# Performance work log

Measured on AMD Instinct MI355X. Metric: run time of the kernel, lower is better.

The kernel has to match this reference:

```python
import jax, jax.numpy as jnp
import numpy as np
import math

QUERY_DIM = 512
FEAT_DIM = 2048
HID_DIM = 512
OUT_DIM = 512
B, L, S, T = 32, 128, 36, 36


def _linear_params(key, d_in, d_out):
    kw, kb = jax.random.split(key)
    scale = 1.0 / math.sqrt(d_in)
    W = jax.random.uniform(kw, (d_in, d_out), jnp.float32, -scale, scale)
    b = jax.random.uniform(kb, (d_out,), jnp.float32, -scale, scale)
    return W, b


def setup_inputs() -> dict:
    key = jax.random.key(0)
    ks = jax.random.split(key, 9)
    query = jax.random.normal(ks[0], (B, L, QUERY_DIM), jnp.float32)
    src = jax.random.normal(ks[1], (B, S, FEAT_DIM), jnp.float32)
    trg = jax.random.normal(ks[2], (B, T, FEAT_DIM), jnp.float32)
    Wq, bq = _linear_params(ks[3], QUERY_DIM, HID_DIM)
    Ws, bs = _linear_params(ks[4], FEAT_DIM, HID_DIM)
    Wt, bt = _linear_params(ks[5], FEAT_DIM, HID_DIM)
    Wsv, bsv = _linear_params(ks[6], FEAT_DIM, HID_DIM)
    Wtv, btv = _linear_params(ks[7], FEAT_DIM, HID_DIM)
    Wo, bo = _linear_params(ks[8], HID_DIM * 2 + QUERY_DIM, OUT_DIM)
    return dict(query=query, src=src, trg=trg,
                Wq=Wq, bq=bq, Ws=Ws, bs=bs, Wt=Wt, bt=bt,
                Wsv=Wsv, bsv=bsv, Wtv=Wtv, btv=btv, Wo=Wo, bo=bo)


def reference(query, src, trg, Wq, bq, Ws, bs, Wt, bt, Wsv, bsv, Wtv, btv, Wo, bo):
    b, l, _ = query.shape
    s = src.shape[1]
    t = trg.shape[1]
    q = query @ Wq + bq                      # (b, l, h)
    s_key = src @ Ws + bs                    # (b, s, h)
    t_key = trg @ Wt + bt                    # (b, t, h)
    # Faithful to torch: s_key.unsqueeze(1) + t_key.unsqueeze(2) -> (b, t, s, h),
    # then labeled 'istk' in the einsum (requires s == t).
    rel_key = (s_key[:, None, :, :] + t_key[:, :, None, :]) * 0.5  # (b, t, s, h)
    weight = jnp.einsum('blk,bstk->blst', q, rel_key) / math.sqrt(HID_DIM)
    weight = jax.nn.softmax(weight.reshape(b, l, s * t), axis=-1).reshape(b, l, s, t)
    s_value = src @ Wsv + bsv                # (b, s, h)
    t_value = trg @ Wtv + btv                # (b, t, h)
    s_ctx = jnp.einsum('blst,bsh->blh', weight, s_value)
    t_ctx = jnp.einsum('blst,bth->blh', weight, t_value)
    x = jnp.concatenate((query, s_ctx, t_ctx), axis=-1)
    return jax.nn.relu(x @ Wo + bo)
```

## Files before the change

### kernel.cpp

```cpp
#include <hip/hip_runtime.h>
#include <hip/hip_bf16.h>
#include <math.h>

#define DEVI __device__ __forceinline__

typedef __attribute__((ext_vector_type(4))) float f32x4;
typedef __attribute__((ext_vector_type(8))) short bf16x8;

DEVI unsigned short f2bf(float f) {
  union { float f; unsigned int u; } v; v.f = f;
  return (unsigned short)((v.u + 0x7FFFu + ((v.u >> 16) & 1u)) >> 16);
}
DEVI float bf2f(unsigned short s) {
  union { unsigned int u; float f; } v; v.u = ((unsigned int)s) << 16; return v.f;
}
DEVI bf16x8 pack8(f32x4 a, f32x4 b) {
  bf16x8 r;
  r[0] = (short)f2bf(a[0]); r[1] = (short)f2bf(a[1]);
  r[2] = (short)f2bf(a[2]); r[3] = (short)f2bf(a[3]);
  r[4] = (short)f2bf(b[0]); r[5] = (short)f2bf(b[1]);
  r[6] = (short)f2bf(b[2]); r[7] = (short)f2bf(b[3]);
  return r;
}
DEVI void gload16(const unsigned short* g, unsigned short* l) {
  __builtin_amdgcn_global_load_lds(
      (const __attribute__((address_space(1))) unsigned int*)g,
      (__attribute__((address_space(3))) unsigned int*)l, 16, 0, 0);
}
#define SBAR() do { asm volatile("" ::: "memory"); \
                    __builtin_amdgcn_s_barrier();  \
                    asm volatile("" ::: "memory"); } while (0)

struct PrepJobs {
  const float* src[9];
  unsigned short* dst[9];
  int K[9];
  int base[9];
  int type[9];
};

__global__ __launch_bounds__(256) void prep(PrepJobs J) {
  __shared__ float t[64][65];
  int tile = blockIdx.x;
  int job = 0;
  while (job < 8 && tile >= J.base[job + 1]) ++job;
  int tl = tile - J.base[job];
  int K = J.K[job];
  if (J.type[job] == 0) {
    int tn = tl & 7, tk = tl >> 3;
    int x = threadIdx.x & 63, y = threadIdx.x >> 6;
    const float* s = J.src[job];
    int k0 = tk * 64, n0 = tn * 64;
#pragma unroll
    for (int yy = y; yy < 64; yy += 4)
      t[yy][x] = s[(size_t)(k0 + yy) * 512 + n0 + x];
    __syncthreads();
    unsigned short* d = J.dst[job];
    int kb = (x >> 3) & 7, ko = x & 7;
#pragma unroll
    for (int yy = y; yy < 64; yy += 4) {
      int n = n0 + yy;
      int kswz = k0 + (((kb + n) & 7) << 3) + ko;
      d[(size_t)n * K + kswz] = f2bf(t[x][yy]);
    }
  } else {
    int nk = K >> 6;
    int rt = tl / nk;
    int r0 = rt * 64, k0 = (tl - rt * nk) * 64;
    int r = threadIdx.x >> 2, kq = threadIdx.x & 3;
    int row = r0 + r;
    const float* s = J.src[job] + (size_t)row * K + k0 + kq * 16;
    f32x4 a0 = *(const f32x4*)s;
    f32x4 a1 = *(const f32x4*)(s + 4);
    f32x4 a2 = *(const f32x4*)(s + 8);
    f32x4 a3 = *(const f32x4*)(s + 12);
    unsigned short* d = J.dst[job] + (size_t)row * K + k0;
    int kb0 = kq * 2;
    *(bf16x8*)(d + ((kb0 + row) & 7) * 8) = pack8(a0, a1);
    *(bf16x8*)(d + ((kb0 + 1 + row) & 7) * 8) = pack8(a2, a3);
  }
}

struct GJob {
  const unsigned short* A0;
  const unsigned short* Bt;
  const float* bias;
  unsigned short* Cb;
  int Astride, Bstride, Cstride, nTilesN, nt, mode, tileBase;
};
struct GBatch { GJob j[7]; int njobs; int swz; };

__global__ __launch_bounds__(512) void gemm_pipe8(GBatch batch) {
  int gt = blockIdx.x;
  if (batch.swz) {
    int cpx = gridDim.x >> 3;
    gt = (blockIdx.x & 7) * cpx + (blockIdx.x >> 3);
  }
  int job = 0;
#pragma unroll
  for (int i = 1; i < 7; ++i)
    if (i < batch.njobs && gt >= batch.j[i].tileBase) job = i;
  GJob J = batch.j[job];
  int tl = gt - J.tileBase;
  int bm = (tl / J.nTilesN) * 128, bn = (tl % J.nTilesN) * 128;

  __shared__ __align__(16) unsigned short La[2][128 * 64];
  __shared__ __align__(16) unsigned short Lb[2][128 * 64];

  int tid = threadIdx.x;
  int wave = tid >> 6, lane = tid & 63;
  int lrow = lane & 15, lq = lane >> 4;
  int wr = (wave >> 1) * 32, wc = (wave & 1) * 64;
  f32x4 acc[2][4] = {};

  int nt = J.nt;

  auto stage_both = [&](int t, int buf) {
    const unsigned short* GA = J.A0 + (size_t)bm * J.Astride + (size_t)(t << 6);
    const unsigned short* GB = J.Bt + (size_t)bn * J.Bstride + (size_t)(t << 6);
#pragma unroll
    for (int p = 0; p < 2; ++p) {
      int s = p * 512 + tid;
      gload16(GA + (size_t)(s >> 3) * J.Astride + (s & 7) * 8,
              &La[buf][(size_t)(p * 512 + wave * 64) * 8]);
    }
#pragma unroll
    for (int p = 0; p < 2; ++p) {
      int s = p * 512 + tid;
      gload16(GB + (size_t)(s >> 3) * J.Bstride + (s & 7) * 8,
              &Lb[buf][(size_t)(p * 512 + wave * 64) * 8]);
    }
  };

  stage_both(0, 0);
  if (nt > 1) stage_both(1, 1);

  for (int t = 0; t < nt; ++t) {
    if (t + 1 < nt) asm volatile("s_waitcnt vmcnt(4)" ::: "memory");
    else            asm volatile("s_waitcnt vmcnt(0)" ::: "memory");
    SBAR();
    int cur = t & 1;
#pragma unroll
    for (int kc = 0; kc < 2; ++kc) {
      int kb = kc * 4 + lq;
      bf16x8 af[2], bv[4];
#pragma unroll
      for (int mi = 0; mi < 2; ++mi) {
        int r = wr + mi * 16 + lrow;
        af[mi] = *(const bf16x8*)&La[cur][r * 64 + ((kb + r) & 7) * 8];
      }
#pragma unroll
      for (int ni = 0; ni < 4; ++ni) {
        int r = wc + ni * 16 + lrow;
        bv[ni] = *(const bf16x8*)&Lb[cur][r * 64 + ((kb + r) & 7) * 8];
      }
#pragma unroll
      for (int mi = 0; mi < 2; ++mi)
#pragma unroll
        for (int ni = 0; ni < 4; ++ni)
          acc[mi][ni] = __builtin_amdgcn_mfma_f32_16x16x32_bf16(af[mi], bv[ni], acc[mi][ni], 0, 0, 0);
    }
    SBAR();
    if (t + 2 < nt) stage_both(t + 2, cur);
  }

#pragma unroll
  for (int mi = 0; mi < 2; ++mi) {
#pragma unroll
    for (int ni = 0; ni < 4; ++ni) {
      int gn = bn + wc + ni * 16 + lrow;
      float bvs = J.bias ? J.bias[gn] : 0.f;
      int gm0 = bm + wr + mi * 16 + lq * 4;
      if (J.mode == 0) {
#pragma unroll
        for (int r = 0; r < 4; ++r)
          J.Cb[(size_t)(gm0 + r) * J.Cstride + gn] = f2bf(acc[mi][ni][r] + bvs);
      } else {
#pragma unroll
        for (int r = 0; r < 4; ++r) {
          int row = gm0 + r;
          int col = (gn & ~63) | (((((gn >> 3) & 7) + row) & 7) << 3) | (gn & 7);
          J.Cb[(size_t)row * J.Cstride + col] = f2bf(acc[mi][ni][r] + bvs);
        }
      }
    }
  }
}

template <int MI, int NI>
__global__ __launch_bounds__(256) void gemm_pipe(GBatch batch) {
  constexpr int BM = MI * 32, BN = NI * 32;
  int gt = blockIdx.x;
  if (batch.swz) {
    int cpx = gridDim.x >> 3;
    gt = (blockIdx.x & 7) * cpx + (blockIdx.x >> 3);
  }
  int job = 0;
#pragma unroll
  for (int i = 1; i < 7; ++i)
    if (i < batch.njobs && gt >= batch.j[i].tileBase) job = i;
  GJob J = batch.j[job];
  int tl = gt - J.tileBase;
  int bm = (tl / J.nTilesN) * BM, bn = (tl % J.nTilesN) * BN;

  __shared__ __align__(16) unsigned short La[2][BM * 64];
  __shared__ __align__(16) unsigned short Lb[2][BN * 64];

  int tid = threadIdx.x;
  int wave = tid >> 6, lane = tid & 63;
  int lrow = lane & 15, lq = lane >> 4;
  int wr = (wave >> 1) * (MI * 16), wc = (wave & 1) * (NI * 16);
  f32x4 acc[MI][NI] = {};

  int nt = J.nt;

  auto stage_both = [&](int t, int buf) {
    const unsigned short* GA = J.A0 + (size_t)bm * J.Astride + (size_t)(t << 6);
    const unsigned short* GB = J.Bt + (size_t)bn * J.Bstride + (size_t)(t << 6);
#pragma unroll
    for (int p = 0; p < MI; ++p) {
      int s = p * 256 + tid;
      gload16(GA + (size_t)(s >> 3) * J.Astride + (s & 7) * 8,
              &La[buf][(size_t)(p * 256 + wave * 64) * 8]);
    }
#pragma unroll
    for (int p = 0; p < NI; ++p) {
      int s = p * 256 + tid;
      gload16(GB + (size_t)(s >> 3) * J.Bstride + (s & 7) * 8,
              &Lb[buf][(size_t)(p * 256 + wave * 64) * 8]);
    }
  };

  stage_both(0, 0);
  if (nt > 1) stage_both(1, 1);

  for (int t = 0; t < nt; ++t) {
    if (t + 1 < nt) {
      if constexpr (MI + NI == 8)      asm volatile("s_waitcnt vmcnt(8)" ::: "memory");
      else if constexpr (MI + NI == 6) asm volatile("s_waitcnt vmcnt(6)" ::: "memory");
      else                             asm volatile("s_waitcnt vmcnt(4)" ::: "memory");
    } else {
      asm volatile("s_waitcnt vmcnt(0)" ::: "memory");
    }
    SBAR();
    int cur = t & 1;
#pragma unroll
    for (int kc = 0; kc < 2; ++kc) {
      int kb = kc * 4 + lq;
      bf16x8 af[MI], bv[NI];
#pragma unroll
      for (int mi = 0; mi < MI; ++mi) {
        int r = wr + mi * 16 + lrow;
        af[mi] = *(const bf16x8*)&La[cur][r * 64 + ((kb + r) & 7) * 8];
      }
#pragma unroll
      for (int ni = 0; ni < NI; ++ni) {
        int r = wc + ni * 16 + lrow;
        bv[ni] = *(const bf16x8*)&Lb[cur][r * 64 + ((kb + r) & 7) * 8];
      }
#pragma unroll
      for (int mi = 0; mi < MI; ++mi)
#pragma unroll
        for (int ni = 0; ni < NI; ++ni)
          acc[mi][ni] = __builtin_amdgcn_mfma_f32_16x16x32_bf16(af[mi], bv[ni], acc[mi][ni], 0, 0, 0);
    }
    SBAR();
    if (t + 2 < nt) stage_both(t + 2, cur);
  }

#pragma unroll
  for (int mi = 0; mi < MI; ++mi) {
#pragma unroll
    for (int ni = 0; ni < NI; ++ni) {
      int gn = bn + wc + ni * 16 + lrow;
      float bvs = J.bias ? J.bias[gn] : 0.f;
      int gm0 = bm + wr + mi * 16 + lq * 4;
      if (J.mode == 0) {
#pragma unroll
        for (int r = 0; r < 4; ++r)
          J.Cb[(size_t)(gm0 + r) * J.Cstride + gn] = f2bf(acc[mi][ni][r] + bvs);
      } else {
#pragma unroll
        for (int r = 0; r < 4; ++r) {
          int row = gm0 + r;
          int col = (gn & ~63) | (((((gn >> 3) & 7) + row) & 7) << 3) | (gn & 7);
          J.Cb[(size_t)row * J.Cstride + col] = f2bf(acc[mi][ni][r] + bvs);
        }
      }
    }
  }
}

__global__ __launch_bounds__(256) void attn_fused(
    const unsigned short* __restrict__ qh, const unsigned short* __restrict__ s_key,
    const unsigned short* __restrict__ t_key, const unsigned short* __restrict__ svp,
    const unsigned short* __restrict__ tvp, const unsigned short* __restrict__ Pb,
    float* __restrict__ out) {
  __shared__ float red[4][3][64][4];
  __shared__ float wlT[2][36][16];
  int b = blockIdx.x, lc = blockIdx.y;
  int tid = threadIdx.x, wave = tid >> 6, lane = tid & 63;
  int lrow = lane & 15, lq = lane >> 4;
  int mat = wave >> 1, kh = wave & 1;
  int row0 = b * 128 + lc * 16;
  const unsigned short* qp = qh + (size_t)row0 * 512;
  const unsigned short* key = (mat ? s_key : t_key) + (size_t)b * 36 * 512;
  f32x4 acc[3] = {};
  for (int kc = kh * 8; kc < kh * 8 + 8; ++kc) {
    int k = kc * 32 + lq * 8;
    bf16x8 af = *(const bf16x8*)(qp + (size_t)lrow * 512 + k);
#pragma unroll
    for (int nf = 0; nf < 3; ++nf) {
      int n = nf * 16 + lrow; if (n > 35) n = 35;
      bf16x8 bv = *(const bf16x8*)(key + (size_t)n * 512 + k);
      acc[nf] = __builtin_amdgcn_mfma_f32_16x16x32_bf16(af, bv, acc[nf], 0, 0, 0);
    }
  }
#pragma unroll
  for (int nf = 0; nf < 3; ++nf)
    *(f32x4*)&red[wave][nf][lane][0] = acc[nf];
  __syncthreads();

  if (kh == 0) {
    const float ccs = 0.022097086912079608f;
    float ex[3][4];
#pragma unroll
    for (int r = 0; r < 4; ++r) {
      float a0 = (red[wave][0][lane][r] + red[wave + 1][0][lane][r]) * ccs;
      float a1 = (red[wave][1][lane][r] + red[wave + 1][1][lane][r]) * ccs;
      float a2 = (lrow < 4)
          ? (red[wave][2][lane][r] + red[wave + 1][2][lane][r]) * ccs : -1e30f;
      float mx = fmaxf(fmaxf(a0, a1), a2);
      for (int s = 1; s < 16; s <<= 1) mx = fmaxf(mx, __shfl_xor(mx, s));
      float e0 = __expf(a0 - mx), e1 = __expf(a1 - mx);
      float e2 = (lrow < 4) ? __expf(a2 - mx) : 0.f;
      float sum = e0 + e1 + e2;
      for (int s = 1; s < 16; s <<= 1) sum += __shfl_xor(sum, s);
      float inv = 1.f / sum;
      ex[0][r] = e0 * inv; ex[1][r] = e1 * inv; ex[2][r] = e2 * inv;
    }
#pragma unroll
    for (int nf = 0; nf < 3; ++nf) {
      int col = nf * 16 + lrow;
      if (col < 36) {
#pragma unroll
        for (int r = 0; r < 4; ++r)
          wlT[mat][col][lq * 4 + r] = ex[nf][r];
      }
    }
  }
  __syncthreads();

  int lgrp = tid >> 6, hgrp = tid & 63;
  float a2[4][8] = {};
#pragma unroll
  for (int m = 0; m < 2; ++m) {
    const unsigned short* V = (m ? tvp : svp) + (size_t)b * 36 * 512;
    for (int j = 0; j < 36; ++j) {
      f32x4 wa = *(const f32x4*)&wlT[m][j][lgrp * 4];
      bf16x8 v = *(const bf16x8*)(V + (size_t)j * 512 + hgrp * 8);
      float vf[8];
#pragma unroll
      for (int hi = 0; hi < 8; ++hi) vf[hi] = bf2f((unsigned short)v[hi]);
#pragma unroll
      for (int li = 0; li < 4; ++li)
#pragma unroll
        for (int hi = 0; hi < 8; ++hi) a2[li][hi] += wa[li] * vf[hi];
    }
  }
#pragma unroll
  for (int li = 0; li < 4; ++li) {
    int R = row0 + lgrp * 4 + li;
    bf16x8 p = *(const bf16x8*)(Pb + (size_t)R * 512 + hgrp * 8);
    float* op = out + (size_t)R * 512 + hgrp * 8;
    f32x4 o0, o1;
#pragma unroll
    for (int hi = 0; hi < 4; ++hi) {
      o0[hi] = fmaxf(bf2f((unsigned short)p[hi]) + a2[li][hi], 0.f);
      o1[hi] = fmaxf(bf2f((unsigned short)p[4 + hi]) + a2[li][4 + hi], 0.f);
    }
    *(f32x4*)op = o0;
    *(f32x4*)(op + 4) = o1;
  }
}

extern "C" void kernel_launch(void* const* d_in, const int* in_sizes, int n_in,
                              void* d_out, int out_size, void* d_ws, size_t ws_size,
                              hipStream_t stream) {
  (void)in_sizes; (void)n_in; (void)out_size; (void)ws_size;
  const float* query = (const float*)d_in[0];
  const float* src   = (const float*)d_in[1];
  const float* trg   = (const float*)d_in[2];
  const float* Wq  = (const float*)d_in[3];  const float* bq  = (const float*)d_in[4];
  const float* Wsk = (const float*)d_in[5];  const float* bs  = (const float*)d_in[6];
  const float* Wtk = (const float*)d_in[7];  const float* bt  = (const float*)d_in[8];
  const float* Wsv = (const float*)d_in[9];  const float* bsv = (const float*)d_in[10];
  const float* Wtv = (const float*)d_in[11]; const float* btv = (const float*)d_in[12];
  const float* Wo  = (const float*)d_in[13]; const float* bo  = (const float*)d_in[14];

  unsigned short* WqT    = (unsigned short*)d_ws;
  unsigned short* WsT    = WqT  + 512 * 512;
  unsigned short* WtT    = WsT  + 512 * 2048;
  unsigned short* WsvT   = WtT  + 512 * 2048;
  unsigned short* WtvT   = WsvT + 512 * 2048;
  unsigned short* WoT    = WtvT + 512 * 2048;
  unsigned short* queryB = WoT  + 512 * 1536;
  unsigned short* srcB   = queryB + 4096 * 512;
  unsigned short* trgB   = srcB + 1152 * 2048;
  unsigned short* qh     = trgB + 1152 * 2048;
  unsigned short* s_key  = qh + 4096 * 512;
  unsigned short* t_key  = s_key + 1152 * 512;
  unsigned short* s_val  = t_key + 1152 * 512;
  unsigned short* t_val  = s_val + 1152 * 512;
  unsigned short* svp    = t_val + 1152 * 512;
  unsigned short* tvp    = svp + 1152 * 512;
  unsigned short* Pb     = tvp + 1152 * 512;
  float* out = (float*)d_out;

  PrepJobs pj;
  const float* psrc[9] = { Wq, Wsk, Wtk, Wsv, Wtv, Wo, query, src, trg };
  unsigned short* pdst[9] = { WqT, WsT, WtT, WsvT, WtvT, WoT, queryB, srcB, trgB };
  int pK[9]    = { 512, 2048, 2048, 2048, 2048, 1536, 512, 2048, 2048 };
  int ptype[9] = { 0, 0, 0, 0, 0, 0, 1, 1, 1 };
  int prows[9] = { 0, 0, 0, 0, 0, 0, 4096, 1152, 1152 };
  int pbase = 0;
  for (int i = 0; i < 9; ++i) {
    pj.src[i] = psrc[i]; pj.dst[i] = pdst[i]; pj.K[i] = pK[i]; pj.type[i] = ptype[i];
    pj.base[i] = pbase;
    pbase += ptype[i] ? (prows[i] / 64) * (pK[i] / 64) : (pK[i] / 64) * 8;
  }
  prep<<<pbase, 256, 0, stream>>>(pj);

  {
    GBatch pb;
    pb.swz = 0;
    int base = 0;
    const unsigned short* Aarr[4] = { srcB, trgB, srcB, trgB };
    const unsigned short* Barr[4] = { WsT, WtT, WsvT, WtvT };
    const float* biasArr[4] = { bs, bt, bsv, btv };
    unsigned short* Carr[4] = { s_key, t_key, s_val, t_val };
    for (int i = 0; i < 4; ++i) {
      GJob& j = pb.j[i];
      j.A0 = Aarr[i]; j.Bt = Barr[i]; j.bias = biasArr[i]; j.Cb = Carr[i];
      j.Astride = 2048; j.Bstride = 2048; j.Cstride = 512;
      j.nTilesN = 4; j.nt = 32; j.mode = (i < 2) ? 0 : 2;
      j.tileBase = base; base += 9 * 4;
    }
    {
      GJob& j = pb.j[4];
      j.A0 = queryB; j.Bt = WqT; j.bias = bq; j.Cb = qh;
      j.Astride = 512; j.Bstride = 512; j.Cstride = 512;
      j.nTilesN = 4; j.nt = 8; j.mode = 0;
      j.tileBase = base; base += 32 * 4;
    }
    {
      GJob& j = pb.j[5];
      j.A0 = queryB; j.Bt = WoT; j.bias = bo; j.Cb = Pb;
      j.Astride = 512; j.Bstride = 1536; j.Cstride = 512;
      j.nTilesN = 4; j.nt = 8; j.mode = 0;
      j.tileBase = base; base += 32 * 4;
    }
    pb.j[6] = pb.j[5]; pb.j[6].tileBase = 0x7fffffff;
    pb.njobs = 6;
    gemm_pipe8<<<base, 512, 0, stream>>>(pb);
  }

  {
    GBatch sb;
    sb.swz = 1;
    GJob& a = sb.j[0];
    a.A0 = s_val; a.Bt = WoT + 512; a.bias = nullptr; a.Cb = svp;
    a.Astride = 512; a.Bstride = 1536; a.Cstride = 512;
    a.nTilesN = 8; a.nt = 8; a.mode = 0; a.tileBase = 0;
    GJob& b2 = sb.j[1];
    b2 = a;
    b2.A0 = t_val; b2.Bt = WoT + 1024; b2.Cb = tvp;
    b2.tileBase = 18 * 8;
    for (int i = 2; i < 7; ++i) { sb.j[i] = b2; sb.j[i].tileBase = 0x7fffffff; }
    sb.njobs = 2;
    gemm_pipe<2, 2><<<288, 256, 0, stream>>>(sb);
  }

  attn_fused<<<dim3(32, 8), 256, 0, stream>>>(qh, s_key, t_key, svp, tvp, Pb, out);
}
```

Baseline: 75.84 us.

## Fuse fp32-to-bf16 activation conversion into GEMM and split attention scoring into stage3

Drops the separate prep pass that converted query/src/trg to swizzled bf16. The projection GEMM now loads fp32 activations into registers, converts them and writes them to LDS, using 64-row tiles with 256 threads. The score/softmax part of the attention kernel moves into a combined launch alongside the value-by-Wo GEMM, writing softmax weights to a workspace for a separate weighted-sum kernel. This saves a full round trip of activation conversion traffic and overlaps the scoring with the small GEMM, at the cost of register-staged A loads and an extra fp32 weights buffer.

```diff
diff --git a/kernel.cpp b/kernel.cpp
--- a/kernel.cpp
+++ b/kernel.cpp
@@ -32,79 +32,57 @@
                     asm volatile("" ::: "memory"); } while (0)
 
 struct PrepJobs {
-  const float* src[9];
-  unsigned short* dst[9];
-  int K[9];
-  int base[9];
-  int type[9];
+  const float* src[6];
+  unsigned short* dst[6];
+  int K[6];
+  int base[6];
 };
 
 __global__ __launch_bounds__(256) void prep(PrepJobs J) {
   __shared__ float t[64][65];
   int tile = blockIdx.x;
   int job = 0;
-  while (job < 8 && tile >= J.base[job + 1]) ++job;
+  while (job < 5 && tile >= J.base[job + 1]) ++job;
   int tl = tile - J.base[job];
   int K = J.K[job];
-  if (J.type[job] == 0) {
-    int tn = tl & 7, tk = tl >> 3;
-    int x = threadIdx.x & 63, y = threadIdx.x >> 6;
-    const float* s = J.src[job];
-    int k0 = tk * 64, n0 = tn * 64;
-#pragma unroll
-    for (int yy = y; yy < 64; yy += 4)
-      t[yy][x] = s[(size_t)(k0 + yy) * 512 + n0 + x];
-    __syncthreads();
-    unsigned short* d = J.dst[job];
-    int kb = (x >> 3) & 7, ko = x & 7;
-#pragma unroll
-    for (int yy = y; yy < 64; yy += 4) {
-      int n = n0 + yy;
-      int kswz = k0 + (((kb + n) & 7) << 3) + ko;
-      d[(size_t)n * K + kswz] = f2bf(t[x][yy]);
-    }
-  } else {
-    int nk = K >> 6;
-    int rt = tl / nk;
-    int r0 = rt * 64, k0 = (tl - rt * nk) * 64;
-    int r = threadIdx.x >> 2, kq = threadIdx.x & 3;
-    int row = r0 + r;
-    const float* s = J.src[job] + (size_t)row * K + k0 + kq * 16;
-    f32x4 a0 = *(const f32x4*)s;
-    f32x4 a1 = *(const f32x4*)(s + 4);
-    f32x4 a2 = *(const f32x4*)(s + 8);
-    f32x4 a3 = *(const f32x4*)(s + 12);
-    unsigned short* d = J.dst[job] + (size_t)row * K + k0;
-    int kb0 = kq * 2;
-    *(bf16x8*)(d + ((kb0 + row) & 7) * 8) = pack8(a0, a1);
-    *(bf16x8*)(d + ((kb0 + 1 + row) & 7) * 8) = pack8(a2, a3);
-  }
-}
-
-struct GJob {
-  const unsigned short* A0;
+  int tn = tl & 7, tk = tl >> 3;
+  int x = threadIdx.x & 63, y = threadIdx.x >> 6;
+  const float* s = J.src[job];
+  int k0 = tk * 64, n0 = tn * 64;
+#pragma unroll
+  for (int yy = y; yy < 64; yy += 4)
+    t[yy][x] = s[(size_t)(k0 + yy) * 512 + n0 + x];
+  __syncthreads();
+  unsigned short* d = J.dst[job];
+  int kb = (x >> 3) & 7, ko = x & 7;
+#pragma unroll
+  for (int yy = y; yy < 64; yy += 4) {
+    int n = n0 + yy;
+    int kswz = k0 + (((kb + n) & 7) << 3) + ko;
+    d[(size_t)n * K + kswz] = f2bf(t[x][yy]);
+  }
+}
+
+struct PJob {
+  const float* Af;
   const unsigned short* Bt;
   const float* bias;
   unsigned short* Cb;
   int Astride, Bstride, Cstride, nTilesN, nt, mode, tileBase;
 };
-struct GBatch { GJob j[7]; int njobs; int swz; };
-
-__global__ __launch_bounds__(512) void gemm_pipe8(GBatch batch) {
+struct PBatch { PJob j[7]; int njobs; };
+
+__global__ __launch_bounds__(256, 3) void gemm_f32a(PBatch batch) {
   int gt = blockIdx.x;
-  if (batch.swz) {
-    int cpx = gridDim.x >> 3;
-    gt = (blockIdx.x & 7) * cpx + (blockIdx.x >> 3);
-  }
   int job = 0;
 #pragma unroll
   for (int i = 1; i < 7; ++i)
     if (i < batch.njobs && gt >= batch.j[i].tileBase) job = i;
-  GJob J = batch.j[job];
+  PJob J = batch.j[job];
   int tl = gt - J.tileBase;
-  int bm = (tl / J.nTilesN) * 128, bn = (tl % J.nTilesN) * 128;
-
-  __shared__ __align__(16) unsigned short La[2][128 * 64];
+  int bm = (tl / J.nTilesN) * 64, bn = (tl % J.nTilesN) * 128;
+
+  __shared__ __align__(16) unsigned short La[2][64 * 64];
   __shared__ __align__(16) unsigned short Lb[2][128 * 64];
 
   int tid = threadIdx.x;
@@ -113,32 +91,38 @@
   int wr = (wave >> 1) * 32, wc = (wave & 1) * 64;
   f32x4 acc[2][4] = {};
 
+  int row_a = tid >> 2, kq = tid & 3;
+  const float* Abase = J.Af + (size_t)(bm + row_a) * J.Astride + kq * 16;
   int nt = J.nt;
 
-  auto stage_both = [&](int t, int buf) {
-    const unsigned short* GA = J.A0 + (size_t)bm * J.Astride + (size_t)(t << 6);
+  f32x4 R[2][4];
+  auto a_load = [&](int t, int s) {
+    const float* p = Abase + (t << 6);
+    R[s][0] = *(const f32x4*)p;       R[s][1] = *(const f32x4*)(p + 4);
+    R[s][2] = *(const f32x4*)(p + 8); R[s][3] = *(const f32x4*)(p + 12);
+  };
+  auto a_write = [&](int s, int buf) {
+    int kb0 = kq * 2;
+    *(bf16x8*)&La[buf][row_a * 64 + ((kb0 + row_a) & 7) * 8]     = pack8(R[s][0], R[s][1]);
+    *(bf16x8*)&La[buf][row_a * 64 + ((kb0 + 1 + row_a) & 7) * 8] = pack8(R[s][2], R[s][3]);
+  };
+  auto b_dma = [&](int t, int buf) {
     const unsigned short* GB = J.Bt + (size_t)bn * J.Bstride + (size_t)(t << 6);
 #pragma unroll
-    for (int p = 0; p < 2; ++p) {
-      int s = p * 512 + tid;
-      gload16(GA + (size_t)(s >> 3) * J.Astride + (s & 7) * 8,
-              &La[buf][(size_t)(p * 512 + wave * 64) * 8]);
-    }
-#pragma unroll
-    for (int p = 0; p < 2; ++p) {
-      int s = p * 512 + tid;
+    for (int p = 0; p < 4; ++p) {
+      int s = p * 256 + tid;
       gload16(GB + (size_t)(s >> 3) * J.Bstride + (s & 7) * 8,
-              &Lb[buf][(size_t)(p * 512 + wave * 64) * 8]);
+              &Lb[buf][(size_t)(p * 256 + wave * 64) * 8]);
     }
   };
 
-  stage_both(0, 0);
-  if (nt > 1) stage_both(1, 1);
+  a_load(0, 0); b_dma(0, 0); a_write(0, 0);
+  if (nt > 1) { a_load(1, 1); b_dma(1, 1); a_write(1, 1); }
+  if (nt > 2) a_load(2, 0);
+  asm volatile("s_waitcnt lgkmcnt(0)" ::: "memory");
+  SBAR();
 
   for (int t = 0; t < nt; ++t) {
-    if (t + 1 < nt) asm volatile("s_waitcnt vmcnt(4)" ::: "memory");
-    else            asm volatile("s_waitcnt vmcnt(0)" ::: "memory");
-    SBAR();
     int cur = t & 1;
 #pragma unroll
     for (int kc = 0; kc < 2; ++kc) {
@@ -161,7 +145,15 @@
           acc[mi][ni] = __builtin_amdgcn_mfma_f32_16x16x32_bf16(af[mi], bv[ni], acc[mi][ni], 0, 0, 0);
     }
     SBAR();
-    if (t + 2 < nt) stage_both(t + 2, cur);
+    if (t + 2 < nt) {
+      a_write(cur, cur);
+      b_dma(t + 2, cur);
+      if (t + 3 < nt) a_load(t + 3, cur ^ 1);
+    } else {
+      asm volatile("s_waitcnt vmcnt(0)" ::: "memory");
+    }
+    asm volatile("s_waitcnt lgkmcnt(0)" ::: "memory");
+    SBAR();
   }
 
 #pragma unroll
@@ -187,167 +179,165 @@
   }
 }
 
-template <int MI, int NI>
-__global__ __launch_bounds__(256) void gemm_pipe(GBatch batch) {
-  constexpr int BM = MI * 32, BN = NI * 32;
-  int gt = blockIdx.x;
-  if (batch.swz) {
-    int cpx = gridDim.x >> 3;
-    gt = (blockIdx.x & 7) * cpx + (blockIdx.x >> 3);
-  }
-  int job = 0;
-#pragma unroll
-  for (int i = 1; i < 7; ++i)
-    if (i < batch.njobs && gt >= batch.j[i].tileBase) job = i;
-  GJob J = batch.j[job];
-  int tl = gt - J.tileBase;
-  int bm = (tl / J.nTilesN) * BM, bn = (tl % J.nTilesN) * BN;
-
-  __shared__ __align__(16) unsigned short La[2][BM * 64];
-  __shared__ __align__(16) unsigned short Lb[2][BN * 64];
-
+struct GJob {
+  const unsigned short* A0;
+  const unsigned short* Bt;
+  unsigned short* Cb;
+  int Astride, Bstride, Cstride, nTilesN, nt, tileBase;
+};
+struct S3Args {
+  GJob g[2];
+  int nGemm;
+  const unsigned short* qh;
+  const unsigned short* s_key;
+  const unsigned short* t_key;
+  float* Wsw;
+  float* Wtw;
+};
+
+__global__ __launch_bounds__(256) void stage3(S3Args A) {
+  __shared__ __align__(16) unsigned char smem[32768];
   int tid = threadIdx.x;
   int wave = tid >> 6, lane = tid & 63;
   int lrow = lane & 15, lq = lane >> 4;
-  int wr = (wave >> 1) * (MI * 16), wc = (wave & 1) * (NI * 16);
-  f32x4 acc[MI][NI] = {};
-
-  int nt = J.nt;
-
-  auto stage_both = [&](int t, int buf) {
-    const unsigned short* GA = J.A0 + (size_t)bm * J.Astride + (size_t)(t << 6);
-    const unsigned short* GB = J.Bt + (size_t)bn * J.Bstride + (size_t)(t << 6);
-#pragma unroll
-    for (int p = 0; p < MI; ++p) {
-      int s = p * 256 + tid;
-      gload16(GA + (size_t)(s >> 3) * J.Astride + (s & 7) * 8,
-              &La[buf][(size_t)(p * 256 + wave * 64) * 8]);
-    }
-#pragma unroll
-    for (int p = 0; p < NI; ++p) {
-      int s = p * 256 + tid;
-      gload16(GB + (size_t)(s >> 3) * J.Bstride + (s & 7) * 8,
-              &Lb[buf][(size_t)(p * 256 + wave * 64) * 8]);
-    }
-  };
-
-  stage_both(0, 0);
-  if (nt > 1) stage_both(1, 1);
-
-  for (int t = 0; t < nt; ++t) {
-    if (t + 1 < nt) {
-      if constexpr (MI + NI == 8)      asm volatile("s_waitcnt vmcnt(8)" ::: "memory");
-      else if constexpr (MI + NI == 6) asm volatile("s_waitcnt vmcnt(6)" ::: "memory");
-      else                             asm volatile("s_waitcnt vmcnt(4)" ::: "memory");
-    } else {
-      asm volatile("s_waitcnt vmcnt(0)" ::: "memory");
-    }
-    SBAR();
-    int cur = t & 1;
-#pragma unroll
-    for (int kc = 0; kc < 2; ++kc) {
-      int kb = kc * 4 + lq;
-      bf16x8 af[MI], bv[NI];
-#pragma unroll
-      for (int mi = 0; mi < MI; ++mi) {
-        int r = wr + mi * 16 + lrow;
-        af[mi] = *(const bf16x8*)&La[cur][r * 64 + ((kb + r) & 7) * 8];
-      }
-#pragma unroll
-      for (int ni = 0; ni < NI; ++ni) {
-        int r = wc + ni * 16 + lrow;
-        bv[ni] = *(const bf16x8*)&Lb[cur][r * 64 + ((kb + r) & 7) * 8];
-      }
-#pragma unroll
-      for (int mi = 0; mi < MI; ++mi)
-#pragma unroll
-        for (int ni = 0; ni < NI; ++ni)
-          acc[mi][ni] = __builtin_amdgcn_mfma_f32_16x16x32_bf16(af[mi], bv[ni], acc[mi][ni], 0, 0, 0);
-    }
-    SBAR();
-    if (t + 2 < nt) stage_both(t + 2, cur);
-  }
-
-#pragma unroll
-  for (int mi = 0; mi < MI; ++mi) {
-#pragma unroll
-    for (int ni = 0; ni < NI; ++ni) {
-      int gn = bn + wc + ni * 16 + lrow;
-      float bvs = J.bias ? J.bias[gn] : 0.f;
-      int gm0 = bm + wr + mi * 16 + lq * 4;
-      if (J.mode == 0) {
+
+  if ((int)blockIdx.x < A.nGemm) {
+    unsigned short* Ls = (unsigned short*)smem;
+    int gt = blockIdx.x;
+    GJob J = (gt >= A.g[1].tileBase) ? A.g[1] : A.g[0];
+    int tl = gt - J.tileBase;
+    int bm = (tl / J.nTilesN) * 64, bn = (tl % J.nTilesN) * 64;
+    int wr = (wave >> 1) * 32, wc = (wave & 1) * 32;
+    f32x4 acc[2][2] = {};
+    int nt = J.nt;
+
+    auto stage_both = [&](int t, int buf) {
+      const unsigned short* GA = J.A0 + (size_t)bm * J.Astride + (size_t)(t << 6);
+      const unsigned short* GB = J.Bt + (size_t)bn * J.Bstride + (size_t)(t << 6);
+#pragma unroll
+      for (int p = 0; p < 2; ++p) {
+        int s = p * 256 + tid;
+        gload16(GA + (size_t)(s >> 3) * J.Astride + (s & 7) * 8,
+                &Ls[(size_t)buf * 4096 + (size_t)(p * 256 + wave * 64) * 8]);
+      }
+#pragma unroll
+      for (int p = 0; p < 2; ++p) {
+        int s = p * 256 + tid;
+        gload16(GB + (size_t)(s >> 3) * J.Bstride + (s & 7) * 8,
+                &Ls[8192 + (size_t)buf * 4096 + (size_t)(p * 256 + wave * 64) * 8]);
+      }
+    };
+
+    stage_both(0, 0);
+    if (nt > 1) stage_both(1, 1);
+
+    for (int t = 0; t < nt; ++t) {
+      if (t + 1 < nt) asm volatile("s_waitcnt vmcnt(4)" ::: "memory");
+      else            asm volatile("s_waitcnt vmcnt(0)" ::: "memory");
+      SBAR();
+      int cur = t & 1;
+#pragma unroll
+      for (int kc = 0; kc < 2; ++kc) {
+        int kb = kc * 4 + lq;
+        bf16x8 af[2], bv[2];
+#pragma unroll
+        for (int mi = 0; mi < 2; ++mi) {
+          int r = wr + mi * 16 + lrow;
+          af[mi] = *(const bf16x8*)&Ls[(size_t)cur * 4096 + r * 64 + ((kb + r) & 7) * 8];
+        }
+#pragma unroll
+        for (int ni = 0; ni < 2; ++ni) {
+          int r = wc + ni * 16 + lrow;
+          bv[ni] = *(const bf16x8*)&Ls[8192 + (size_t)cur * 4096 + r * 64 + ((kb + r) & 7) * 8];
+        }
+#pragma unroll
+        for (int mi = 0; mi < 2; ++mi)
+#pragma unroll
+          for (int ni = 0; ni < 2; ++ni)
+            acc[mi][ni] = __builtin_amdgcn_mfma_f32_16x16x32_bf16(af[mi], bv[ni], acc[mi][ni], 0, 0, 0);
+      }
+      SBAR();
+      if (t + 2 < nt) stage_both(t + 2, cur);
+    }
+#pragma unroll
+    for (int mi = 0; mi < 2; ++mi) {
+#pragma unroll
+      for (int ni = 0; ni < 2; ++ni) {
+        int gn = bn + wc + ni * 16 + lrow;
+        int gm0 = bm + wr + mi * 16 + lq * 4;
 #pragma unroll
         for (int r = 0; r < 4; ++r)
-          J.Cb[(size_t)(gm0 + r) * J.Cstride + gn] = f2bf(acc[mi][ni][r] + bvs);
-      } else {
-#pragma unroll
-        for (int r = 0; r < 4; ++r) {
-          int row = gm0 + r;
-          int col = (gn & ~63) | (((((gn >> 3) & 7) + row) & 7) << 3) | (gn & 7);
-          J.Cb[(size_t)row * J.Cstride + col] = f2bf(acc[mi][ni][r] + bvs);
+          J.Cb[(size_t)(gm0 + r) * J.Cstride + gn] = f2bf(acc[mi][ni][r]);
+      }
+    }
+  } else {
+    float (*red)[3][64][4] = (float(*)[3][64][4])smem;
+    int bid2 = blockIdx.x - A.nGemm;
+    int b = bid2 >> 3, lc = bid2 & 7;
+    int mat = wave >> 1, kh = wave & 1;
+    int row0 = b * 128 + lc * 16;
+    const unsigned short* qp = A.qh + (size_t)row0 * 512;
+    const unsigned short* key = (mat ? A.s_key : A.t_key) + (size_t)b * 36 * 512;
+    f32x4 acc[3] = {};
+    for (int kc = kh * 8; kc < kh * 8 + 8; ++kc) {
+      int k = kc * 32 + lq * 8;
+      bf16x8 af = *(const bf16x8*)(qp + (size_t)lrow * 512 + k);
+#pragma unroll
+      for (int nf = 0; nf < 3; ++nf) {
+        int n = nf * 16 + lrow; if (n > 35) n = 35;
+        bf16x8 bv = *(const bf16x8*)(key + (size_t)n * 512 + k);
+        acc[nf] = __builtin_amdgcn_mfma_f32_16x16x32_bf16(af, bv, acc[nf], 0, 0, 0);
+      }
+    }
+#pragma unroll
+    for (int nf = 0; nf < 3; ++nf)
+      *(f32x4*)&red[wave][nf][lane][0] = acc[nf];
+    __syncthreads();
+
+    if (kh == 0) {
+      const float ccs = 0.022097086912079608f;
+      float ex[3][4];
+#pragma unroll
+      for (int r = 0; r < 4; ++r) {
+        float a0 = (red[wave][0][lane][r] + red[wave + 1][0][lane][r]) * ccs;
+        float a1 = (red[wave][1][lane][r] + red[wave + 1][1][lane][r]) * ccs;
+        float a2 = (lrow < 4)
+            ? (red[wave][2][lane][r] + red[wave + 1][2][lane][r]) * ccs : -1e30f;
+        float mx = fmaxf(fmaxf(a0, a1), a2);
+        for (int s = 1; s < 16; s <<= 1) mx = fmaxf(mx, __shfl_xor(mx, s));
+        float e0 = __expf(a0 - mx), e1 = __expf(a1 - mx);
+        float e2 = (lrow < 4) ? __expf(a2 - mx) : 0.f;
+        float sum = e0 + e1 + e2;
+        for (int s = 1; s < 16; s <<= 1) sum += __shfl_xor(sum, s);
+        float inv = 1.f / sum;
+        ex[0][r] = e0 * inv; ex[1][r] = e1 * inv; ex[2][r] = e2 * inv;
+      }
+      float* W = mat ? A.Wtw : A.Wsw;
+#pragma unroll
+      for (int nf = 0; nf < 3; ++nf) {
+        int col = nf * 16 + lrow;
+        if (col < 36) {
+#pragma unroll
+          for (int r = 0; r < 4; ++r)
+            W[(size_t)(row0 + lq * 4 + r) * 36 + col] = ex[nf][r];
         }
       }
     }
   }
 }
 
-__global__ __launch_bounds__(256) void attn_fused(
-    const unsigned short* __restrict__ qh, const unsigned short* __restrict__ s_key,
-    const unsigned short* __restrict__ t_key, const unsigned short* __restrict__ svp,
-    const unsigned short* __restrict__ tvp, const unsigned short* __restrict__ Pb,
-    float* __restrict__ out) {
-  __shared__ float red[4][3][64][4];
+__global__ __launch_bounds__(256) void wsum(
+    const float* __restrict__ Wsw, const float* __restrict__ Wtw,
+    const unsigned short* __restrict__ svp, const unsigned short* __restrict__ tvp,
+    const unsigned short* __restrict__ Pb, float* __restrict__ out) {
   __shared__ float wlT[2][36][16];
   int b = blockIdx.x, lc = blockIdx.y;
-  int tid = threadIdx.x, wave = tid >> 6, lane = tid & 63;
-  int lrow = lane & 15, lq = lane >> 4;
-  int mat = wave >> 1, kh = wave & 1;
+  int tid = threadIdx.x;
   int row0 = b * 128 + lc * 16;
-  const unsigned short* qp = qh + (size_t)row0 * 512;
-  const unsigned short* key = (mat ? s_key : t_key) + (size_t)b * 36 * 512;
-  f32x4 acc[3] = {};
-  for (int kc = kh * 8; kc < kh * 8 + 8; ++kc) {
-    int k = kc * 32 + lq * 8;
-    bf16x8 af = *(const bf16x8*)(qp + (size_t)lrow * 512 + k);
-#pragma unroll
-    for (int nf = 0; nf < 3; ++nf) {
-      int n = nf * 16 + lrow; if (n > 35) n = 35;
-      bf16x8 bv = *(const bf16x8*)(key + (size_t)n * 512 + k);
-      acc[nf] = __builtin_amdgcn_mfma_f32_16x16x32_bf16(af, bv, acc[nf], 0, 0, 0);
-    }
-  }
-#pragma unroll
-  for (int nf = 0; nf < 3; ++nf)
-    *(f32x4*)&red[wave][nf][lane][0] = acc[nf];
-  __syncthreads();
-
-  if (kh == 0) {
-    const float ccs = 0.022097086912079608f;
-    float ex[3][4];
-#pragma unroll
-    for (int r = 0; r < 4; ++r) {
-      float a0 = (red[wave][0][lane][r] + red[wave + 1][0][lane][r]) * ccs;
-      float a1 = (red[wave][1][lane][r] + red[wave + 1][1][lane][r]) * ccs;
-      float a2 = (lrow < 4)
-          ? (red[wave][2][lane][r] + red[wave + 1][2][lane][r]) * ccs : -1e30f;
-      float mx = fmaxf(fmaxf(a0, a1), a2);
-      for (int s = 1; s < 16; s <<= 1) mx = fmaxf(mx, __shfl_xor(mx, s));
-      float e0 = __expf(a0 - mx), e1 = __expf(a1 - mx);
-      float e2 = (lrow < 4) ? __expf(a2 - mx) : 0.f;
-      float sum = e0 + e1 + e2;
-      for (int s = 1; s < 16; s <<= 1) sum += __shfl_xor(sum, s);
-      float inv = 1.f / sum;
-      ex[0][r] = e0 * inv; ex[1][r] = e1 * inv; ex[2][r] = e2 * inv;
-    }
-#pragma unroll
-    for (int nf = 0; nf < 3; ++nf) {
-      int col = nf * 16 + lrow;
-      if (col < 36) {
-#pragma unroll
-        for (int r = 0; r < 4; ++r)
-          wlT[mat][col][lq * 4 + r] = ex[nf][r];
-      }
-    }
+  for (int i = tid; i < 2 * 16 * 36; i += 256) {
+    int m = i / 576, rem = i - m * 576;
+    int l = rem / 36, j = rem - l * 36;
+    wlT[m][j][l] = (m ? Wtw : Wsw)[(size_t)(row0 + l) * 36 + j];
   }
   __syncthreads();
 
@@ -404,10 +394,7 @@
   unsigned short* WsvT   = WtT  + 512 * 2048;
   unsigned short* WtvT   = WsvT + 512 * 2048;
   unsigned short* WoT    = WtvT + 512 * 2048;
-  unsigned short* queryB = WoT  + 512 * 1536;
-  unsigned short* srcB   = queryB + 4096 * 512;
-  unsigned short* trgB   = srcB + 1152 * 2048;
-  unsigned short* qh     = trgB + 1152 * 2048;
+  unsigned short* qh     = WoT  + 512 * 1536;
   unsigned short* s_key  = qh + 4096 * 512;
   unsigned short* t_key  = s_key + 1152 * 512;
   unsigned short* s_val  = t_key + 1152 * 512;
@@ -415,71 +402,70 @@
   unsigned short* svp    = t_val + 1152 * 512;
   unsigned short* tvp    = svp + 1152 * 512;
   unsigned short* Pb     = tvp + 1152 * 512;
+  float* Wsw = (float*)(Pb + 4096 * 512);
+  float* Wtw = Wsw + 4096 * 36;
   float* out = (float*)d_out;
 
   PrepJobs pj;
-  const float* psrc[9] = { Wq, Wsk, Wtk, Wsv, Wtv, Wo, query, src, trg };
-  unsigned short* pdst[9] = { WqT, WsT, WtT, WsvT, WtvT, WoT, queryB, srcB, trgB };
-  int pK[9]    = { 512, 2048, 2048, 2048, 2048, 1536, 512, 2048, 2048 };
-  int ptype[9] = { 0, 0, 0, 0, 0, 0, 1, 1, 1 };
-  int prows[9] = { 0, 0, 0, 0, 0, 0, 4096, 1152, 1152 };
+  const float* psrc[6] = { Wq, Wsk, Wtk, Wsv, Wtv, Wo };
+  unsigned short* pdst[6] = { WqT, WsT, WtT, WsvT, WtvT, WoT };
+  int pK[6] = { 512, 2048, 2048, 2048, 2048, 1536 };
   int pbase = 0;
-  for (int i = 0; i < 9; ++i) {
-    pj.src[i] = psrc[i]; pj.dst[i] = pdst[i]; pj.K[i] = pK[i]; pj.type[i] = ptype[i];
+  for (int i = 0; i < 6; ++i) {
+    pj.src[i] = psrc[i]; pj.dst[i] = pdst[i]; pj.K[i] = pK[i];
     pj.base[i] = pbase;
-    pbase += ptype[i] ? (prows[i] / 64) * (pK[i] / 64) : (pK[i] / 64) * 8;
+    pbase += (pK[i] / 64) * 8;
   }
   prep<<<pbase, 256, 0, stream>>>(pj);
 
   {
-    GBatch pb;
-    pb.swz = 0;
+    PBatch pb;
     int base = 0;
-    const unsigned short* Aarr[4] = { srcB, trgB, srcB, trgB };
+    const float* Aarr[4] = { src, trg, src, trg };
     const unsigned short* Barr[4] = { WsT, WtT, WsvT, WtvT };
     const float* biasArr[4] = { bs, bt, bsv, btv };
     unsigned short* Carr[4] = { s_key, t_key, s_val, t_val };
     for (int i = 0; i < 4; ++i) {
-      GJob& j = pb.j[i];
-      j.A0 = Aarr[i]; j.Bt = Barr[i]; j.bias = biasArr[i]; j.Cb = Carr[i];
+      PJob& j = pb.j[i];
+      j.Af = Aarr[i]; j.Bt = Barr[i]; j.bias = biasArr[i]; j.Cb = Carr[i];
       j.Astride = 2048; j.Bstride = 2048; j.Cstride = 512;
       j.nTilesN = 4; j.nt = 32; j.mode = (i < 2) ? 0 : 2;
-      j.tileBase = base; base += 9 * 4;
+      j.tileBase = base; base += 18 * 4;
     }
     {
-      GJob& j = pb.j[4];
-      j.A0 = queryB; j.Bt = WqT; j.bias = bq; j.Cb = qh;
+      PJob& j = pb.j[4];
+      j.Af = query; j.Bt = WqT; j.bias = bq; j.Cb = qh;
       j.Astride = 512; j.Bstride = 512; j.Cstride = 512;
       j.nTilesN = 4; j.nt = 8; j.mode = 0;
-      j.tileBase = base; base += 32 * 4;
+      j.tileBase = base; base += 64 * 4;
     }
     {
-      GJob& j = pb.j[5];
-      j.A0 = queryB; j.Bt = WoT; j.bias = bo; j.Cb = Pb;
+      PJob& j = pb.j[5];
+      j.Af = query; j.Bt = WoT; j.bias = bo; j.Cb = Pb;
       j.Astride = 512; j.Bstride = 1536; j.Cstride = 512;
       j.nTilesN = 4; j.nt = 8; j.mode = 0;
-      j.tileBase = base; base += 32 * 4;
+      j.tileBase = base; base += 64 * 4;
     }
     pb.j[6] = pb.j[5]; pb.j[6].tileBase = 0x7fffffff;
     pb.njobs = 6;
-    gemm_pipe8<<<base, 512, 0, stream>>>(pb);
+    gemm_f32a<<<base, 256, 0, stream>>>(pb);
   }
 
   {
-    GBatch sb;
-    sb.swz = 1;
-    GJob& a = sb.j[0];
-    a.A0 = s_val; a.Bt = WoT + 512; a.bias = nullptr; a.Cb = svp;
+    S3Args sa;
+    GJob& a = sa.g[0];
+    a.A0 = s_val; a.Bt = WoT + 512; a.Cb = svp;
     a.Astride = 512; a.Bstride = 1536; a.Cstride = 512;
-    a.nTilesN = 8; a.nt = 8; a.mode = 0; a.tileBase = 0;
-    GJob& b2 = sb.j[1];
+    a.nTilesN = 8; a.nt = 8; a.tileBase = 0;
+    GJob& b2 = sa.g[1];
     b2 = a;
     b2.A0 = t_val; b2.Bt = WoT + 1024; b2.Cb = tvp;
     b2.tileBase = 18 * 8;
-    for (int i = 2; i < 7; ++i) { sb.j[i] = b2; sb.j[i].tileBase = 0x7fffffff; }
-    sb.njobs = 2;
-    gemm_pipe<2, 2><<<288, 256, 0, stream>>>(sb);
-  }
-
-  attn_fused<<<dim3(32, 8), 256, 0, stream>>>(qh, s_key, t_key, svp, tvp, Pb, out);
-}
+    sa.nGemm = 288;
+    sa.qh = qh; sa.s_key = s_key; sa.t_key = t_key;
+    sa.Wsw = Wsw; sa.Wtw = Wtw;
+    stage3<<<288 + 256, 256, 0, stream>>>(sa);
+  }
+
+  wsum<<<dim3(32, 8), 256, 0, stream>>>(Wsw, Wtw, svp, tvp, Pb, out);
+}
```

Result: slower. 81.93 us (+8.0%).
